# Performance work log

Hardware: AMD Instinct MI355X
Metric: run time of the kernel (lower is better)

The kernel has to match this reference:

```python
import jax, jax.numpy as jnp
import numpy as np

D, D_r, B, G, I = 1024, 256, 4, 8, 2
Ng = D // G                      # 128 groups
P = (2 * I + 1) * G              # 40 = local window width

# modular overlapping-window index map, shape [Ng, P]
_base = np.arange(-I * G, (I + 1) * G) % D
IDX = jnp.asarray(np.stack([( _base + i * G) % D for i in range(Ng)], axis=0))


def setup_inputs() -> dict:
    key = jax.random.key(0)
    kx, kwi, kbi, kwo = jax.random.split(key, 4)
    x = jax.random.normal(kx, (4096, D), dtype=jnp.float32)
    Wi = jax.random.normal(kwi, (B, D_r, 2 * P), dtype=jnp.float32) * 0.05
    bi = jax.random.normal(kbi, (B, D_r), dtype=jnp.float32) * 0.05
    Wo = jax.random.normal(kwo, (B, G, D_r), dtype=jnp.float32) * 0.05
    return {"x": x, "Wi": Wi, "bi": bi, "Wo": Wo}


def reference(x, Wi, bi, Wo):
    # x: [N, D]; Wi: [B, D_r, 2P]; bi: [B, D_r]; Wo: [B, G, D_r]
    xg = x[..., IDX]                               # [N, Ng, P] gathered once (x is constant across stages)
    z = x
    for i in range(B):
        zg = z[..., IDX]                           # [N, Ng, P]
        y = jnp.concatenate([xg, zg], axis=-1)     # [N, Ng, 2P]
        h = jnp.tanh(jnp.einsum('ngp,rp->ngr', y, Wi[i]) + bi[i])   # [N, Ng, D_r]
        zi = jnp.einsum('ngr,gr->ngg2', h, Wo[i].T.T) if False else jnp.einsum('ngr,cr->ngc', h, Wo[i])  # [N, Ng, G]
        z = zi.reshape(*z.shape[:-1], D)           # flatten group dim back to D
    return z
```

## Files before the change

### kernel.cpp

```cpp
#include <hip/hip_runtime.h>
#include <hip/hip_fp16.h>

#define D_ 1024
#define C2LOG2E 2.8853900817779268f

typedef __fp16   fp16x2 __attribute__((ext_vector_type(2)));
typedef _Float16 h4 __attribute__((ext_vector_type(4)));
typedef _Float16 h8 __attribute__((ext_vector_type(8)));
typedef float    f4 __attribute__((ext_vector_type(4)));

#define MFMA32(A, B, C) __builtin_amdgcn_mfma_f32_16x16x32_f16(A, B, C, 0, 0, 0)
#define MFMA16(A, B, C) __builtin_amdgcn_mfma_f32_16x16x16f16(A, B, C, 0, 0, 0)

__global__ void prep_all(const float* __restrict__ Wi, const float* __restrict__ bi,
                         const float* __restrict__ Wo,
                         h8* __restrict__ Wi16, h4* __restrict__ Wo2) {
    int t = blockIdx.x * 256 + threadIdx.x;
    if (t < 12288) {
        int p16 = t & 15;
        int chunk = (t >> 4) % 12;
        int rt = ((t >> 4) / 12) & 15;
        int st = t / 3072;
        int r = rt * 16 + p16;
        h8 v = {0, 0, 0, 0, 0, 0, 0, 0};
        if (chunk < 10) {
            const float* s = Wi + ((size_t)(st * 256 + r) * 80 + chunk * 8);
#pragma unroll
            for (int j = 0; j < 8; ++j) v[j] = (_Float16)(C2LOG2E * s[j]);
        } else if (chunk == 10) {
            v[0] = (_Float16)(C2LOG2E * bi[st * 256 + r]);
        }
        Wi16[t] = v;
    } else {
        int u = t - 12288;
        if (u >= 4096) return;
        int lane = u & 63;
        int s = (u >> 6) & 1;
        int kc = (u >> 7) & 7;
        int st = u >> 10;
        int p16 = lane & 15, q = lane >> 4;
        h4 v = {0, 0, 0, 0};
        if (p16 < 8) {
            const float* src = Wo + ((size_t)(st * 8 + p16) * 256 + kc * 32 + s * 16 + q * 4);
#pragma unroll
            for (int j = 0; j < 4; ++j) v[j] = (_Float16)src[j];
        }
        Wo2[u] = v;
    }
}

__device__ __forceinline__ h4 tanh4(const f4 a) {
    const __half2 ONE  = __float2half2_rn(1.0f);
    const __half2 MTWO = __float2half2_rn(-2.0f);
    union { h4 v; fp16x2 h[2]; __half2 hh[2]; } u;
    u.h[0] = __builtin_amdgcn_cvt_pkrtz(a[0], a[1]);
    u.h[1] = __builtin_amdgcn_cvt_pkrtz(a[2], a[3]);
#pragma unroll
    for (int i = 0; i < 2; ++i) {
        __half2 e = h2exp2(u.hh[i]);
        __half2 r = h2rcp(__hadd2(e, ONE));
        u.hh[i] = __hfma2(r, MTWO, ONE);
    }
    return u.v;
}

__global__ __launch_bounds__(256, 2) void ldrfm8(
    const float* __restrict__ x,
    const h8* __restrict__ Wi16,
    const h4* __restrict__ Wo2,
    float* __restrict__ out)
{
    __shared__ h8 xr[4][136];
    __shared__ h8 zr[4][136];
    __shared__ h8 cpad[8][16];

    const int tid = threadIdx.x;
    const int w = tid >> 6, lane = tid & 63;
    const int p16 = lane & 15, q = lane >> 4;
    const int row = blockIdx.x * 4 + w;

    if (lane < 16) {
        h8 v = {0, 0, 0, 0, 0, 0, 0, 0};
        if ((lane & 1) == 0) v[0] = (_Float16)1.0f;
        cpad[lane >> 1][lane & 1] = v;
    }

    {
        const f4* xp = (const f4*)(x + (size_t)row * D_) + lane * 4;
        f4 v0 = xp[0], v1 = xp[1], v2 = xp[2], v3 = xp[3];
        union { h8 v; fp16x2 h[4]; } a, b;
        a.h[0] = __builtin_amdgcn_cvt_pkrtz(v0[0], v0[1]);
        a.h[1] = __builtin_amdgcn_cvt_pkrtz(v0[2], v0[3]);
        a.h[2] = __builtin_amdgcn_cvt_pkrtz(v1[0], v1[1]);
        a.h[3] = __builtin_amdgcn_cvt_pkrtz(v1[2], v1[3]);
        b.h[0] = __builtin_amdgcn_cvt_pkrtz(v2[0], v2[1]);
        b.h[1] = __builtin_amdgcn_cvt_pkrtz(v2[2], v2[3]);
        b.h[2] = __builtin_amdgcn_cvt_pkrtz(v3[0], v3[1]);
        b.h[3] = __builtin_amdgcn_cvt_pkrtz(v3[2], v3[3]);
        xr[w][2 * lane + 2] = a.v; xr[w][2 * lane + 3] = b.v;
        zr[w][2 * lane + 2] = a.v; zr[w][2 * lane + 3] = b.v;
        if (lane == 63) {
            xr[w][0] = a.v; xr[w][1] = b.v; zr[w][0] = a.v; zr[w][1] = b.v;
        }
        if (lane == 0) {
            xr[w][130] = a.v; xr[w][131] = b.v; zr[w][130] = a.v; zr[w][131] = b.v;
        }
    }

    const h8* b0p = &xr[w][p16 + q];
    const h8* b1p = (q == 0) ? &xr[w][p16 + 4]
                             : &zr[w][p16 + q - 1];
    const h8* b2p = (q < 2) ? &zr[w][p16 + 3 + q]
                            : (const h8*)&cpad[0][q - 2];
    _Float16* zwp = (_Float16*)&zr[w][p16 + 2] + q * 4;
    float* op = out + (size_t)row * D_ + p16 * 8 + q * 4;

    const f4 FZ = {0.f, 0.f, 0.f, 0.f};

#pragma unroll 1
    for (int st = 0; st < 4; ++st) {
        const h8* WiS = Wi16 + st * 3072;
        const h4* WoS = Wo2 + st * 1024;

        f4 acc2[8];
#pragma unroll
        for (int i = 0; i < 8; ++i) acc2[i] = FZ;

#pragma unroll 1
        for (int kc = 0; kc < 8; ++kc) {
            const h8* wp0 = WiS + ((2 * kc) * 12 + q) * 16 + p16;
            const h8* wp1 = WiS + ((2 * kc + 1) * 12 + q) * 16 + p16;
            h8 A00 = wp0[0], A01 = wp0[64], A02 = wp0[128];
            h8 A10 = wp1[0], A11 = wp1[64], A12 = wp1[128];
            h4 B20 = WoS[(kc * 2 + 0) * 64 + lane];
            h4 B21 = WoS[(kc * 2 + 1) * 64 + lane];

#pragma unroll
            for (int pt = 0; pt < 8; ++pt) {
                h8 b0 = *(const h8*)((const char*)b0p + pt * 256);
                h8 b1 = *(const h8*)((const char*)b1p + pt * 256);
                h8 b2 = *(const h8*)((const char*)b2p + pt * 256);
                f4 a0 = MFMA32(A00, b0, FZ);
                a0 = MFMA32(A01, b1, a0);
                a0 = MFMA32(A02, b2, a0);
                f4 a1 = MFMA32(A10, b0, FZ);
                a1 = MFMA32(A11, b1, a1);
                a1 = MFMA32(A12, b2, a1);
                h4 h0 = tanh4(a0);
                h4 h1 = tanh4(a1);
                acc2[pt] = MFMA16(B20, h0, acc2[pt]);
                acc2[pt] = MFMA16(B21, h1, acc2[pt]);
            }
        }

        if (st < 3) {
#pragma unroll
            for (int pt = 0; pt < 8; ++pt) {
                if (q < 2) {
                    union { h4 v; fp16x2 h[2]; } zv;
                    zv.h[0] = __builtin_amdgcn_cvt_pkrtz(acc2[pt][0], acc2[pt][1]);
                    zv.h[1] = __builtin_amdgcn_cvt_pkrtz(acc2[pt][2], acc2[pt][3]);
                    *(h4*)((char*)zwp + pt * 256) = zv.v;
                    if (pt == 0 && p16 < 2)
                        *(h4*)((char*)zwp + pt * 256 + 2048) = zv.v;
                    if (pt == 7 && p16 >= 14)
                        *(h4*)((char*)zwp + pt * 256 - 2048) = zv.v;
                }
            }
        } else {
#pragma unroll
            for (int pt = 0; pt < 8; ++pt) {
                if (q < 2) *(f4*)(op + pt * 128) = acc2[pt];
            }
        }
    }
}

extern "C" void kernel_launch(void* const* d_in, const int* in_sizes, int n_in,
                              void* d_out, int out_size, void* d_ws, size_t ws_size,
                              hipStream_t stream) {
    const float* x  = (const float*)d_in[0];
    const float* Wi = (const float*)d_in[1];
    const float* bi = (const float*)d_in[2];
    const float* Wo = (const float*)d_in[3];
    float* out = (float*)d_out;

    h8* Wi16 = (h8*)d_ws;
    h4* Wo2  = (h4*)(Wi16 + 12288);

    prep_all<<<64, 256, 0, stream>>>(Wi, bi, Wo, Wi16, Wo2);

    int nrows = in_sizes[0] / D_;
    ldrfm8<<<nrows / 4, 256, 0, stream>>>(x, Wi16, Wo2, out);
}
```

Before: 208.8 us.

## Split each row across two waves, fold tanh into sigmoid via Wo rowsum

Rewrites tanh(a) as 1-2*sigmoid(2a), pre-scaling Wo by -2 and seeding the accumulator with the Wo row sums so each activation needs one fewer FMA. Each row is now split across two waves (half the columns each), and blocks handle 2 rows instead of 4, with a double-buffered z in shared memory and block barriers between stages. The loop order is changed to iterate over all 16 r-chunks per column tile with one accumulator, which cuts register pressure; launch bounds are raised for higher occupancy. The cost is more Wi/Wo fragment reloads per row (streamed inside the inner loop) and __syncthreads per stage.

```diff
diff --git a/kernel.cpp b/kernel.cpp
--- a/kernel.cpp
+++ b/kernel.cpp
@@ -14,7 +14,8 @@
 
 __global__ void prep_all(const float* __restrict__ Wi, const float* __restrict__ bi,
                          const float* __restrict__ Wo,
-                         h8* __restrict__ Wi16, h4* __restrict__ Wo2) {
+                         h8* __restrict__ Wi16, h4* __restrict__ Wo2m,
+                         float* __restrict__ rowsum) {
     int t = blockIdx.x * 256 + threadIdx.x;
     if (t < 12288) {
         int p16 = t & 15;
@@ -31,9 +32,8 @@
             v[0] = (_Float16)(C2LOG2E * bi[st * 256 + r]);
         }
         Wi16[t] = v;
-    } else {
+    } else if (t < 16384) {
         int u = t - 12288;
-        if (u >= 4096) return;
         int lane = u & 63;
         int s = (u >> 6) & 1;
         int kc = (u >> 7) & 7;
@@ -43,49 +43,60 @@
         if (p16 < 8) {
             const float* src = Wo + ((size_t)(st * 8 + p16) * 256 + kc * 32 + s * 16 + q * 4);
 #pragma unroll
-            for (int j = 0; j < 4; ++j) v[j] = (_Float16)src[j];
-        }
-        Wo2[u] = v;
-    }
-}
-
-__device__ __forceinline__ h4 tanh4(const f4 a) {
-    const __half2 ONE  = __float2half2_rn(1.0f);
-    const __half2 MTWO = __float2half2_rn(-2.0f);
+            for (int j = 0; j < 4; ++j) v[j] = (_Float16)(-2.f * src[j]);
+        }
+        Wo2m[u] = v;
+    } else {
+        int u = t - 16384;
+        if (u < 64) {
+            int st = u >> 4, c = u & 15;
+            float s = 0.f;
+            if (c < 8) {
+                const float* src = Wo + (size_t)(st * 8 + c) * 256;
+                for (int k = 0; k < 256; ++k) s += src[k];
+            }
+            rowsum[u] = s;
+        }
+    }
+}
+
+__device__ __forceinline__ h4 sig4(const f4 a) {
+    const __half2 ONE = __float2half2_rn(1.0f);
     union { h4 v; fp16x2 h[2]; __half2 hh[2]; } u;
     u.h[0] = __builtin_amdgcn_cvt_pkrtz(a[0], a[1]);
     u.h[1] = __builtin_amdgcn_cvt_pkrtz(a[2], a[3]);
 #pragma unroll
     for (int i = 0; i < 2; ++i) {
         __half2 e = h2exp2(u.hh[i]);
-        __half2 r = h2rcp(__hadd2(e, ONE));
-        u.hh[i] = __hfma2(r, MTWO, ONE);
+        u.hh[i] = h2rcp(__hadd2(e, ONE));
     }
     return u.v;
 }
 
-__global__ __launch_bounds__(256, 2) void ldrfm8(
+__global__ __launch_bounds__(256, 8) void ldrfm9(
     const float* __restrict__ x,
     const h8* __restrict__ Wi16,
-    const h4* __restrict__ Wo2,
+    const h4* __restrict__ Wo2m,
+    const float* __restrict__ rowsum,
     float* __restrict__ out)
 {
-    __shared__ h8 xr[4][136];
-    __shared__ h8 zr[4][136];
+    __shared__ h8 xr[2][136];
+    __shared__ h8 zb[2][2][136];
     __shared__ h8 cpad[8][16];
 
     const int tid = threadIdx.x;
     const int w = tid >> 6, lane = tid & 63;
     const int p16 = lane & 15, q = lane >> 4;
-    const int row = blockIdx.x * 4 + w;
-
-    if (lane < 16) {
+    const int lrow = w >> 1, half = w & 1;
+    const int row = blockIdx.x * 2 + lrow;
+
+    if (w == 0 && lane < 16) {
         h8 v = {0, 0, 0, 0, 0, 0, 0, 0};
         if ((lane & 1) == 0) v[0] = (_Float16)1.0f;
         cpad[lane >> 1][lane & 1] = v;
     }
 
-    {
+    if (half == 0) {
         const f4* xp = (const f4*)(x + (size_t)row * D_) + lane * 4;
         f4 v0 = xp[0], v1 = xp[1], v2 = xp[2], v3 = xp[3];
         union { h8 v; fp16x2 h[4]; } a, b;
@@ -97,82 +108,76 @@
         b.h[1] = __builtin_amdgcn_cvt_pkrtz(v2[2], v2[3]);
         b.h[2] = __builtin_amdgcn_cvt_pkrtz(v3[0], v3[1]);
         b.h[3] = __builtin_amdgcn_cvt_pkrtz(v3[2], v3[3]);
-        xr[w][2 * lane + 2] = a.v; xr[w][2 * lane + 3] = b.v;
-        zr[w][2 * lane + 2] = a.v; zr[w][2 * lane + 3] = b.v;
+        xr[lrow][2 * lane + 2] = a.v;    xr[lrow][2 * lane + 3] = b.v;
+        zb[0][lrow][2 * lane + 2] = a.v; zb[0][lrow][2 * lane + 3] = b.v;
         if (lane == 63) {
-            xr[w][0] = a.v; xr[w][1] = b.v; zr[w][0] = a.v; zr[w][1] = b.v;
+            xr[lrow][0] = a.v; xr[lrow][1] = b.v;
+            zb[0][lrow][0] = a.v; zb[0][lrow][1] = b.v;
         }
         if (lane == 0) {
-            xr[w][130] = a.v; xr[w][131] = b.v; zr[w][130] = a.v; zr[w][131] = b.v;
-        }
-    }
-
-    const h8* b0p = &xr[w][p16 + q];
-    const h8* b1p = (q == 0) ? &xr[w][p16 + 4]
-                             : &zr[w][p16 + q - 1];
-    const h8* b2p = (q < 2) ? &zr[w][p16 + 3 + q]
-                            : (const h8*)&cpad[0][q - 2];
-    _Float16* zwp = (_Float16*)&zr[w][p16 + 2] + q * 4;
-    float* op = out + (size_t)row * D_ + p16 * 8 + q * 4;
-
+            xr[lrow][130] = a.v; xr[lrow][131] = b.v;
+            zb[0][lrow][130] = a.v; zb[0][lrow][131] = b.v;
+        }
+    }
+    __syncthreads();
+
+    const char* xbase = (const char*)&xr[lrow][0] + half * 1024;
+    const char* b0p = xbase + (p16 + q) * 16;
+    float* op = out + (size_t)row * D_ + half * 512 + p16 * 8 + q * 4;
     const f4 FZ = {0.f, 0.f, 0.f, 0.f};
 
 #pragma unroll 1
     for (int st = 0; st < 4; ++st) {
         const h8* WiS = Wi16 + st * 3072;
-        const h4* WoS = Wo2 + st * 1024;
-
-        f4 acc2[8];
-#pragma unroll
-        for (int i = 0; i < 8; ++i) acc2[i] = FZ;
+        const h4* WoS = Wo2m + st * 1024;
+        const f4 rs = *(const f4*)(rowsum + st * 16 + q * 4);
+
+        const char* zcur = (const char*)&zb[st & 1][lrow][0] + half * 1024;
+        char* znxt = (char*)&zb[(st + 1) & 1][lrow][0] + half * 1024;
+        const char* b1p = (q == 0) ? (xbase + (p16 + 4) * 16)
+                                   : (zcur + (p16 + q - 1) * 16);
+        const char* b2p = (q < 2) ? (zcur + (p16 + 3 + q) * 16)
+                                  : ((const char*)&cpad[half * 4][q - 2]);
+        char* zw = znxt + (p16 + 2) * 16 + q * 8;
 
 #pragma unroll 1
-        for (int kc = 0; kc < 8; ++kc) {
-            const h8* wp0 = WiS + ((2 * kc) * 12 + q) * 16 + p16;
-            const h8* wp1 = WiS + ((2 * kc + 1) * 12 + q) * 16 + p16;
-            h8 A00 = wp0[0], A01 = wp0[64], A02 = wp0[128];
-            h8 A10 = wp1[0], A11 = wp1[64], A12 = wp1[128];
-            h4 B20 = WoS[(kc * 2 + 0) * 64 + lane];
-            h4 B21 = WoS[(kc * 2 + 1) * 64 + lane];
-
-#pragma unroll
-            for (int pt = 0; pt < 8; ++pt) {
-                h8 b0 = *(const h8*)((const char*)b0p + pt * 256);
-                h8 b1 = *(const h8*)((const char*)b1p + pt * 256);
-                h8 b2 = *(const h8*)((const char*)b2p + pt * 256);
-                f4 a0 = MFMA32(A00, b0, FZ);
-                a0 = MFMA32(A01, b1, a0);
-                a0 = MFMA32(A02, b2, a0);
-                f4 a1 = MFMA32(A10, b0, FZ);
-                a1 = MFMA32(A11, b1, a1);
-                a1 = MFMA32(A12, b2, a1);
-                h4 h0 = tanh4(a0);
-                h4 h1 = tanh4(a1);
-                acc2[pt] = MFMA16(B20, h0, acc2[pt]);
-                acc2[pt] = MFMA16(B21, h1, acc2[pt]);
+        for (int ptl = 0; ptl < 4; ++ptl) {
+            h8 b0 = *(const h8*)(b0p + ptl * 256);
+            h8 b1 = *(const h8*)(b1p + ptl * 256);
+            h8 b2 = *(const h8*)(b2p + ptl * 256);
+            f4 acc = rs;
+
+            const h8* Ap = WiS + q * 16 + p16;
+            const h4* Bp = WoS + lane;
+#pragma unroll 2
+            for (int ph = 0; ph < 16; ++ph) {
+                h8 A0 = Ap[0], A1 = Ap[64], A2 = Ap[128];
+                h4 Bf = Bp[0];
+                f4 a = MFMA32(A0, b0, FZ);
+                a = MFMA32(A1, b1, a);
+                a = MFMA32(A2, b2, a);
+                h4 r = sig4(a);
+                acc = MFMA16(Bf, r, acc);
+                Ap += 192;
+                Bp += 64;
             }
-        }
-
-        if (st < 3) {
-#pragma unroll
-            for (int pt = 0; pt < 8; ++pt) {
+
+            if (st < 3) {
                 if (q < 2) {
                     union { h4 v; fp16x2 h[2]; } zv;
-                    zv.h[0] = __builtin_amdgcn_cvt_pkrtz(acc2[pt][0], acc2[pt][1]);
-                    zv.h[1] = __builtin_amdgcn_cvt_pkrtz(acc2[pt][2], acc2[pt][3]);
-                    *(h4*)((char*)zwp + pt * 256) = zv.v;
-                    if (pt == 0 && p16 < 2)
-                        *(h4*)((char*)zwp + pt * 256 + 2048) = zv.v;
-                    if (pt == 7 && p16 >= 14)
-                        *(h4*)((char*)zwp + pt * 256 - 2048) = zv.v;
+                    zv.h[0] = __builtin_amdgcn_cvt_pkrtz(acc[0], acc[1]);
+                    zv.h[1] = __builtin_amdgcn_cvt_pkrtz(acc[2], acc[3]);
+                    *(h4*)(zw + ptl * 256) = zv.v;
+                    if (half == 0 && ptl == 0 && p16 < 2)
+                        *(h4*)(zw + ptl * 256 + 2048) = zv.v;
+                    if (half == 1 && ptl == 3 && p16 >= 14)
+                        *(h4*)(zw + ptl * 256 - 2048) = zv.v;
                 }
+            } else {
+                if (q < 2) *(f4*)(op + ptl * 128) = acc;
             }
-        } else {
-#pragma unroll
-            for (int pt = 0; pt < 8; ++pt) {
-                if (q < 2) *(f4*)(op + pt * 128) = acc2[pt];
-            }
-        }
+        }
+        if (st < 3) __syncthreads();
     }
 }
 
@@ -186,10 +191,11 @@
     float* out = (float*)d_out;
 
     h8* Wi16 = (h8*)d_ws;
-    h4* Wo2  = (h4*)(Wi16 + 12288);
-
-    prep_all<<<64, 256, 0, stream>>>(Wi, bi, Wo, Wi16, Wo2);
+    h4* Wo2m = (h4*)((char*)d_ws + 196608);
+    float* rowsum = (float*)((char*)d_ws + 229376);
+
+    prep_all<<<65, 256, 0, stream>>>(Wi, bi, Wo, Wi16, Wo2m, rowsum);
 
     int nrows = in_sizes[0] / D_;
-    ldrfm8<<<nrows / 4, 256, 0, stream>>>(x, Wi16, Wo2, out);
-}
+    ldrfm9<<<nrows / 2, 256, 0, stream>>>(x, Wi16, Wo2m, rowsum, out);
+}
```

Result: slower. 321.2 us (+53.8%).
